# Optimization experiments

Measured on AMD Instinct MI355X. Metric: run time of the kernel, lower is better.

The kernel has to match this reference:

```python
import jax, jax.numpy as jnp
import numpy as np
from jax import lax

N = 200; E = 3200; HID = 64; NH = 16; OUT = 2 * HID; CAT = NH * OUT  # CAT = 2048
ALPHA = 0.2


def _gat(h, e_attr, adj, n2n, W, a_s, a_d, a_e, We, concat):
    # edge-feature-aware GAT head: logits from Wh_i, Wh_j and projected node2node feats
    Nn = h.shape[0]
    Wh = h @ W                                       # [N, out]
    ee = ((n2n @ We) @ a_e).reshape(Nn, Nn)          # [N, N] edge-feature term
    logits = jax.nn.leaky_relu((Wh @ a_s)[:, None] + (Wh @ a_d)[None, :] + ee,
                               negative_slope=ALPHA)
    logits = jnp.where(adj > 0, logits, -1e9)        # mask to graph structure
    att = jax.nn.softmax(logits, axis=1)
    h2 = att @ Wh
    if concat:
        h2 = jax.nn.elu(h2)
    return h2, jax.nn.elu(e_attr @ We)               # updated node + edge features


def _edge_pool(x, eidx, e, w, b):
    # static-shape edge pooling: score edges, gate nodes by mean incident score
    src, dst = eidx[0], eidx[1]
    s = jax.nn.sigmoid(jnp.concatenate([x[src], x[dst], e], axis=1) @ w + b)  # [E]
    deg = jax.ops.segment_sum(jnp.ones_like(s), src, num_segments=x.shape[0])
    ns = jax.ops.segment_sum(s, src, num_segments=x.shape[0]) / (deg + 1e-6)
    return x * ns[:, None], e * s[:, None]


def _gpool(x, w, b):
    # GlobalAttention: gate_nn = Linear+Sigmoid, softmax over nodes, weighted sum
    gate = jax.nn.softmax(jax.nn.sigmoid(x @ w + b), axis=0)  # [N, 1]
    return jnp.sum(gate * x, axis=0, keepdims=True)           # [1, D]


def _adj_n2n(Nn, eidx, eattr):
    # vectorized version of the per-edge Python loop in _get_adj_node2node
    src, dst = eidx[0], eidx[1]
    adj = jnp.zeros((Nn, Nn), eattr.dtype).at[src, dst].set(1.0)
    n2n = jnp.zeros((Nn * Nn, eattr.shape[1]), eattr.dtype).at[src * Nn + dst].set(eattr)
    return adj, n2n


def _lstm_dir(x, Wih, Whh, b):
    # one LSTM direction over seq x [T, Din] (PyTorch i,f,g,o gate order)
    Hh = Whh.shape[1]
    def step(carry, xt):
        h, c = carry
        g = xt @ Wih.T + h @ Whh.T + b
        i, f, gg, o = jnp.split(g, 4)
        c = jax.nn.sigmoid(f) * c + jax.nn.sigmoid(i) * jnp.tanh(gg)
        h = jax.nn.sigmoid(o) * jnp.tanh(c)
        return (h, c), h
    (_, _), ys = lax.scan(step, (jnp.zeros(Hh, x.dtype), jnp.zeros(Hh, x.dtype)), x)
    return ys


def setup_inputs():
    key = jax.random.key(0)
    ks = iter(jax.random.split(key, 64))
    def rn(shape, scale=0.05):
        return jax.random.normal(next(ks), shape, jnp.float32) * scale
    inp = {}
    for g in (1, 2):
        eidx = jax.random.randint(next(ks), (2, E), 0, N)
        eattr = rn((E, HID), 1.0)
        adj, n2n = _adj_n2n(N, eidx, eattr)
        inp['features%d' % g] = rn((N, HID), 1.0)
        inp['edge_index%d' % g] = eidx
        inp['edgesAttr%d' % g] = eattr
        inp['adjacency%d' % g] = adj
        inp['node2node%d' % g] = n2n
    inp.update(dict(
        W_h=rn((HID, HID)),
        W_gat=rn((NH, HID, OUT)), a_src=rn((NH, OUT)), a_dst=rn((NH, OUT)),
        a_e=rn((NH, OUT)), We_gat=rn((NH, HID, OUT)),
        W_out=rn((CAT, OUT)), ao_src=rn((OUT,)), ao_dst=rn((OUT,)), ao_e=rn((OUT,)),
        We_out=rn((CAT, OUT)),
        ep1_w=rn((3 * CAT,)), ep1_b=rn(()),
        ep2_w=rn((3 * OUT,)), ep2_b=rn(()),
        g1_w=rn((HID, 1)), g1_b=rn((1,)),
        g2_w=rn((CAT, 1)), g2_b=rn((1,)),
        g3_w=rn((OUT, 1)), g3_b=rn((1,)),
        Wih0=rn((2, 512, 35 * HID)), Whh0=rn((2, 512, 128)), b0=rn((2, 512)),
        Wih1=rn((2, 512, 256)), Whh1=rn((2, 512, 128)), b1=rn((2, 512)),
        fc_w=rn((256, 2)), fc_b=rn((2,)),
    ))
    return inp


def reference(features1, features2, edge_index1, edge_index2, edgesAttr1, edgesAttr2,
              adjacency1, adjacency2, node2node1, node2node2,
              W_h, W_gat, a_src, a_dst, a_e, We_gat,
              W_out, ao_src, ao_dst, ao_e, We_out,
              ep1_w, ep1_b, ep2_w, ep2_b,
              g1_w, g1_b, g2_w, g2_b, g3_w, g3_b,
              Wih0, Whh0, b0, Wih1, Whh1, b1, fc_w, fc_b):
    def graph(feat, eidx, eattr, adj, n2n):
        h = jax.nn.elu(feat @ W_h)                              # SingleNodeAttentionLayer
        hs = [_gpool(h, g1_w, g1_b)]
        outs = [_gat(h, eattr, adj, n2n, W_gat[i], a_src[i], a_dst[i], a_e[i],
                     We_gat[i], True) for i in range(NH)]
        h = jnp.concatenate([o[0] for o in outs], axis=1)       # [N, 2048]
        eattr = jnp.concatenate([o[1] for o in outs], axis=1)   # [E, 2048]
        h, eattr = _edge_pool(h, eidx, eattr, ep1_w, ep1_b)
        hs.append(_gpool(h, g2_w, g2_b))
        adj2, n2n2 = _adj_n2n(h.shape[0], eidx, eattr)          # dense [N*N, 2048]
        h, eattr = _gat(h, eattr, adj2, n2n2, W_out, ao_src, ao_dst, ao_e, We_out, False)
        h, eattr = _edge_pool(h, eidx, eattr, ep2_w, ep2_b)
        hs.append(_gpool(h, g3_w, g3_b))
        return jnp.concatenate(hs, axis=1)                      # [1, 35*HID]

    h1 = graph(features1, edge_index1, edgesAttr1, adjacency1, node2node1)
    h2 = graph(features2, edge_index2, edgesAttr2, adjacency2, node2node2)
    x = jnp.concatenate([h1, h2], axis=0)                       # seq [2, 2240]
    for Wih, Whh, b in ((Wih0, Whh0, b0), (Wih1, Whh1, b1)):
        f = _lstm_dir(x, Wih[0], Whh[0], b[0])
        r = _lstm_dir(x[::-1], Wih[1], Whh[1], b[1])[::-1]
        x = jnp.concatenate([f, r], axis=1)                     # [2, 256]
    logits = x[-1] @ fc_w + fc_b
    return jax.nn.softmax(logits)[None, :]                      # [1, nclass]
```

## Files before the change

### kernel.cpp

```cpp
#include <hip/hip_runtime.h>
#include <math.h>

#define DI static __device__ __forceinline__

DI float eluf(float x){ return x > 0.f ? x : expm1f(x); }
DI float lreluf(float x){ return x > 0.f ? x : 0.2f*x; }
DI float sigmf(float x){ return 1.f/(1.f+expf(-x)); }

typedef unsigned short u16;
typedef unsigned int   u32;
typedef __attribute__((ext_vector_type(8))) short short8_t;
typedef __attribute__((ext_vector_type(4))) float f32x4;

DI u16 bf16rne(float f){
  u32 u = __float_as_uint(f);
  u += 0x7fffu + ((u>>16)&1u);
  return (u16)(u>>16);
}

DI f32x4 bmfma(short8_t a, short8_t b, f32x4 c){
  return __builtin_amdgcn_mfma_f32_16x16x32_bf16(a, b, c, 0, 0, 0);
}

constexpr int N=200, E=3200, HID=64, NH=16, OUTD=128, CAT=2048, SEQD=2240;

constexpr int OH0   = 0;
constexpr int OWH   = OH0 + N*HID;
constexpr int OASN  = OWH + NH*N*OUTD;
constexpr int OADN  = OASN + NH*N;
constexpr int OH1   = OADN + NH*N;
constexpr int OXW1  = OH1 + N*CAT;
constexpr int OXW2  = OXW1 + 256;
constexpr int OEW1  = OXW2 + 256;
constexpr int OS1   = OEW1 + E;
constexpr int ODEG1 = OS1 + E;
constexpr int OSS1  = ODEG1 + 256;
constexpr int ORAW1 = OSS1 + 256;
constexpr int OWH2  = ORAW1 + 256;
constexpr int OAS2  = OWH2 + N*OUTD;
constexpr int OAD2  = OAS2 + 256;
constexpr int OEWV  = OAD2 + 256;
constexpr int OH2B  = OEWV + E;
constexpr int OXS2  = OH2B + N*OUTD;
constexpr int OXD2  = OXS2 + 256;
constexpr int ODEG2 = OXD2 + 256;
constexpr int OSS2  = ODEG2 + 256;
constexpr int ORAW2 = OSS2 + 256;
constexpr int ORAW3 = ORAW2 + 256;
constexpr int PGF   = ORAW3 + 256;
constexpr int GLOBF = 10624;
constexpr int TOTF  = GLOBF + 2*PGF;

__device__ __attribute__((aligned(16))) float G_F[TOTF];
__device__ float G_E2PART[(size_t)4*2*E*OUTD];
__device__ float G_EDOTH[2*NH*E];
__device__ float G_WHHT[2*2*128*512];
__device__ int   G_PIDX[2*N*N];
__device__ __attribute__((aligned(16))) u16 G_WGAT_T[NH*OUTD*HID];
__device__ __attribute__((aligned(16))) u16 G_WOUT_T[OUTD*CAT];
__device__ __attribute__((aligned(16))) u16 G_EATTR_BF[2*E*HID];

DI float* gf(int g){ return G_F + GLOBF + (size_t)g*PGF; }
DI float* gwe_ae(){ return G_F; }
DI float* gv_e(){ return G_F + 1024; }
DI float* gy0(){ return G_F + 3072; }
DI float* gy1(){ return G_F + 3584; }
DI float* gxseq(){ return G_F + 4096; }
DI float* gxg(){ return G_F + 8576; }
DI int*   gpidx(int g){ return G_PIDX + g*N*N; }

struct GraphIn {
  const float *feat, *eattr, *adj, *n2n;
  const int   *eidx;
};

struct Params {
  GraphIn g[2];
  const float *W_h, *W_gat, *a_src, *a_dst, *a_e, *We_gat;
  const float *W_out, *ao_src, *ao_dst, *ao_e, *We_out;
  const float *ep1_w, *ep1_b, *ep2_w, *ep2_b;
  const float *g1_w, *g1_b, *g2_w, *g2_b, *g3_w, *g3_b;
  const float *Wih0, *Whh0, *b0, *Wih1, *Whh1, *b1, *fc_w, *fc_b;
  float *out;
};

constexpr int ZPG  = 2*E + 1024;
constexpr int IB_Z = (2*ZPG+255)/256;
constexpr int IB_C = (2*N*N+255)/256;
constexpr int IB_D = (2*2*512*128)/256;
constexpr int IB_E = (NH*HID+CAT+3)/4;
constexpr int IB_H = (2*N+3)/4;
constexpr int IB_W1 = (NH*OUTD*HID)/256;
constexpr int IB_W2 = (OUTD*CAT)/256;
constexpr int IB_EA = (2*E*HID)/256;
__global__ void k_init(Params P){
  int b = blockIdx.x, tid = threadIdx.x;
  if (b < IB_Z){
    int i = b*256 + tid;
    if (i < 2*ZPG){
      int g = i/ZPG, r = i%ZPG;
      int addr = r<E ? OEW1+r : (r<2*E ? OEWV+(r-E) :
                 (r<2*E+512 ? ODEG1+(r-2*E) : ODEG2+(r-2*E-512)));
      gf(g)[addr] = 0.f;
    }
  } else if (b < IB_Z+IB_C){
    int i = (b-IB_Z)*256 + tid; if (i < 2*N*N) G_PIDX[i] = -1;
  } else if (b < IB_Z+IB_C+IB_D){
    int idx = (b-IB_Z-IB_C)*256 + tid;
    int l = idx >> 17;
    int r = idx & 131071;
    int d = r >> 16;
    int r2 = r & 65535;
    int gate = r2 & 511;
    int k = r2 >> 9;
    const float* Whh = l ? P.Whh1 : P.Whh0;
    G_WHHT[idx] = Whh[((size_t)d*512+gate)*128 + k];
  } else if (b < IB_Z+IB_C+IB_D+IB_E){
    int gid = (b-IB_Z-IB_C-IB_D)*4 + (tid>>6);
    int lane = tid & 63;
    if (gid < NH*HID){
      int h = gid/HID, c = gid%HID;
      const float* W = P.We_gat + (size_t)(h*HID+c)*OUTD;
      const float* a = P.a_e + h*OUTD;
      float acc = 0.f;
      for (int o=lane;o<OUTD;o+=64) acc += W[o]*a[o];
      for (int off=32;off>0;off>>=1) acc += __shfl_down(acc,off);
      if (lane==0) gwe_ae()[gid] = acc;
    } else if (gid < NH*HID+CAT){
      int c = gid - NH*HID;
      const float* W = P.We_out + (size_t)c*OUTD;
      float acc = 0.f;
      for (int o=lane;o<OUTD;o+=64) acc += W[o]*P.ao_e[o];
      for (int off=32;off>0;off>>=1) acc += __shfl_down(acc,off);
      if (lane==0) gv_e()[c] = acc;
    }
  } else if (b < IB_Z+IB_C+IB_D+IB_E+IB_H){
    int unit = (b-IB_Z-IB_C-IB_D-IB_E)*4 + (tid>>6);
    if (unit >= 2*N) return;
    int g = unit / N, n = unit % N, c = tid & 63;
    const float* feat = P.g[g].feat;
    float acc = 0.f;
    for (int k=0;k<HID;k++) acc += feat[n*HID+k]*P.W_h[k*HID+c];
    float v = eluf(acc);
    float* f = gf(g);
    f[OH0 + n*HID + c] = v;
    float r = v*P.g1_w[c];
    for (int off=32;off>0;off>>=1) r += __shfl_down(r,off);
    if (c==0) f[ORAW1+n] = r;
  } else if (b < IB_Z+IB_C+IB_D+IB_E+IB_H+IB_W1){
    int i = (b-(IB_Z+IB_C+IB_D+IB_E+IB_H))*256 + tid;
    int h = i>>13, o = (i>>6)&127, c = i&63;
    G_WGAT_T[i] = bf16rne(P.We_gat[(size_t)(h*HID+c)*OUTD + o]);
  } else if (b < IB_Z+IB_C+IB_D+IB_E+IB_H+IB_W1+IB_W2){
    int i = (b-(IB_Z+IB_C+IB_D+IB_E+IB_H+IB_W1))*256 + tid;
    int n = i>>11, q = i&2047;
    G_WOUT_T[i] = bf16rne(P.We_out[(size_t)q*OUTD + n]);
  } else {
    int i = (b-(IB_Z+IB_C+IB_D+IB_E+IB_H+IB_W1+IB_W2))*256 + tid;
    int g = i >= E*HID ? 1 : 0;
    G_EATTR_BF[i] = bf16rne(P.g[g].eattr[i - g*E*HID]);
  }
}

__global__ void k_edoth(Params P){
  int b = blockIdx.x, tid = threadIdx.x;
  int g = b / (E/16);
  int e0 = (b % (E/16)) * 16;
  __shared__ float ea[16][HID+1];
  __shared__ float wa[16][HID+1];
  {
    int row = tid >> 4, c0 = (tid & 15)*4;
    float4 v = *(const float4*)&P.g[g].eattr[(size_t)(e0+row)*HID + c0];
    ea[row][c0]=v.x; ea[row][c0+1]=v.y; ea[row][c0+2]=v.z; ea[row][c0+3]=v.w;
    float4 w = *(const float4*)&gwe_ae()[row*HID + c0];
    wa[row][c0]=w.x; wa[row][c0+1]=w.y; wa[row][c0+2]=w.z; wa[row][c0+3]=w.w;
  }
  __syncthreads();
  int h = tid >> 4, el = tid & 15;
  float acc = 0.f;
  #pragma unroll
  for (int c=0;c<HID;c++) acc += ea[el][c]*wa[h][c];
  G_EDOTH[((size_t)g*NH + h)*E + e0 + el] = acc;
}

__global__ void k_Wh(Params P){
  int n = blockIdx.x, h = blockIdx.y, g = blockIdx.z, o = threadIdx.x;
  float* f = gf(g);
  if (h == NH){
    if (n != 0) return;
    __shared__ float att[N];
    __shared__ float sb[128];
    for (int j = o; j < N; j += 128) att[j] = sigmf(f[ORAW1+j] + P.g1_b[0]);
    __syncthreads();
    float m = -3e38f;
    for (int j = o; j < N; j += 128) m = fmaxf(m, att[j]);
    sb[o] = m; __syncthreads();
    for (int s=64;s>0;s>>=1){ if (o<s) sb[o]=fmaxf(sb[o],sb[o+s]); __syncthreads(); }
    m = sb[0]; __syncthreads();
    float ss = 0.f;
    for (int j = o; j < N; j += 128){ float e = expf(att[j]-m); ss += e; }
    sb[o] = ss; __syncthreads();
    for (int s=64;s>0;s>>=1){ if (o<s) sb[o]+=sb[o+s]; __syncthreads(); }
    float inv = 1.f/sb[0]; __syncthreads();
    for (int j = o; j < N; j += 128) att[j] = expf(att[j]-m)*inv;
    __syncthreads();
    if (o < HID){
      float acc = 0.f;
      for (int j=0;j<N;j++) acc += att[j]*f[OH0 + j*HID + o];
      gxseq()[g*SEQD + o] = acc;
    }
    return;
  }
  __shared__ float hs[HID];
  __shared__ float sred[128], dred[128];
  if (o < HID) hs[o] = f[OH0 + n*HID + o];
  __syncthreads();
  const float* W = P.W_gat + (size_t)h*HID*OUTD + o;
  float acc = 0.f;
  for (int c=0;c<HID;c++) acc += hs[c]*W[(size_t)c*OUTD];
  f[OWH + ((size_t)h*N + n)*OUTD + o] = acc;
  sred[o] = acc*P.a_src[h*OUTD+o];
  dred[o] = acc*P.a_dst[h*OUTD+o];
  __syncthreads();
  for (int s=64;s>0;s>>=1){ if (o<s){ sred[o]+=sred[o+s]; dred[o]+=dred[o+s]; } __syncthreads(); }
  if (o==0){ f[OASN+h*N+n]=sred[0]; f[OADN+h*N+n]=dred[0]; }
}

__global__ void k_att1(Params P){
  int nb = blockIdx.x, h = blockIdx.y, g = blockIdx.z, tid = threadIdx.x;
  int n0 = nb*4;
  __shared__ float z[4][N];
  __shared__ float red[128];
  __shared__ float sinv[4];
  float* f = gf(g);
  const float* adj = P.g[g].adj;
  const int* pidx = gpidx(g);
  const float* edoth = G_EDOTH + ((size_t)g*NH + h)*E;
  const float* adn = f + OADN + h*N;
  for (int i=0;i<4;i++){
    float asn = f[OASN + h*N + n0+i];
    for (int j = tid; j < N; j += 128){
      float a = adj[(n0+i)*N + j];
      float zz;
      if (a > 0.f){
        int p = pidx[(n0+i)*N + j];
        float ee = (p >= 0) ? edoth[p] : 0.f;
        zz = lreluf(asn + adn[j] + ee);
      } else zz = -1e9f;
      z[i][j] = zz;
    }
  }
  __syncthreads();
  for (int i=0;i<4;i++){
    float m = -3e38f;
    for (int j = tid; j < N; j += 128) m = fmaxf(m, z[i][j]);
    red[tid] = m; __syncthreads();
    for (int s=64;s>0;s>>=1){ if (tid<s) red[tid]=fmaxf(red[tid],red[tid+s]); __syncthreads(); }
    m = red[0]; __syncthreads();
    float ssum = 0.f;
    for (int j = tid; j < N; j += 128){ float e = expf(z[i][j]-m); z[i][j]=e; ssum += e; }
    red[tid] = ssum; __syncthreads();
    for (int s=64;s>0;s>>=1){ if (tid<s) red[tid]+=red[tid+s]; __syncthreads(); }
    if (tid==0) sinv[i] = 1.f/red[0];
    __syncthreads();
  }
  const float* wh = f + OWH + (size_t)h*N*OUTD;
  float a0=0.f,a1=0.f,a2=0.f,a3=0.f;
  for (int j=0;j<N;j++){
    float w = wh[(size_t)j*OUTD + tid];
    a0 += z[0][j]*w; a1 += z[1][j]*w; a2 += z[2][j]*w; a3 += z[3][j]*w;
  }
  f[OH1 + (size_t)(n0+0)*CAT + h*OUTD + tid] = eluf(a0*sinv[0]);
  f[OH1 + (size_t)(n0+1)*CAT + h*OUTD + tid] = eluf(a1*sinv[1]);
  f[OH1 + (size_t)(n0+2)*CAT + h*OUTD + tid] = eluf(a2*sinv[2]);
  f[OH1 + (size_t)(n0+3)*CAT + h*OUTD + tid] = eluf(a3*sinv[3]);
}

__global__ void k_xw1(Params P){
  int n = blockIdx.x, g = blockIdx.y, tid = threadIdx.x;
  __shared__ float s1b[256], s2b[256], s3b[256];
  float* f = gf(g);
  const float* x = f + OH1 + (size_t)n*CAT;
  float a1 = 0.f, a2 = 0.f, a3 = 0.f;
  for (int c = tid; c < CAT; c += 256){
    float xv = x[c];
    a1 += xv*P.ep1_w[c];
    a2 += xv*P.ep1_w[CAT+c];
    a3 += xv*P.g2_w[c];
  }
  s1b[tid]=a1; s2b[tid]=a2; s3b[tid]=a3; __syncthreads();
  for (int s=128;s>0;s>>=1){
    if (tid<s){ s1b[tid]+=s1b[tid+s]; s2b[tid]+=s2b[tid+s]; s3b[tid]+=s3b[tid+s]; }
    __syncthreads();
  }
  if (tid==0){ f[OXW1+n]=s1b[0]; f[OXW2+n]=s2b[0]; f[ORAW2+n]=s3b[0]; }
}

__global__ void k_s1(Params P){
  int e = blockIdx.x*256 + threadIdx.x, g = blockIdx.y;
  if (e >= E) return;
  float* f = gf(g);
  const int* ei = P.g[g].eidx;
  int s = ei[e], d = ei[E+e];
  float v = sigmf(f[OXW1+s] + f[OXW2+d] + f[OEW1+e] + P.ep1_b[0]);
  f[OS1+e] = v;
  atomicAdd(&f[OSS1+s], v);
  atomicAdd(&f[ODEG1+s], 1.f);
}

__global__ void k_pairs(Params P){
  int e = blockIdx.x*256 + threadIdx.x, g = blockIdx.y;
  if (e >= E) return;
  const int* ei = P.g[g].eidx;
  atomicMax(&gpidx(g)[ei[e]*N + ei[E+e]], e);
}

__global__ void k_gpool_out(Params P, int xoff, int D, int odeg, int rawoff,
                            const float* b, int outoff){
  int cb = blockIdx.x, g = blockIdx.y, tid = threadIdx.x;
  __shared__ float att[N];
  __shared__ float sb[256];
  float* f = gf(g);
  for (int n = tid; n < N; n += 256){
    float sc = f[odeg+256+n]/(f[odeg+n]+1e-6f);
    att[n] = sigmf(f[rawoff+n]*sc + b[0]);
  }
  __syncthreads();
  float m = -3e38f;
  for (int n = tid; n < N; n += 256) m = fmaxf(m, att[n]);
  sb[tid] = m; __syncthreads();
  for (int s=128;s>0;s>>=1){ if (tid<s) sb[tid]=fmaxf(sb[tid],sb[tid+s]); __syncthreads(); }
  m = sb[0]; __syncthreads();
  float ss = 0.f;
  for (int n = tid; n < N; n += 256){ float e = expf(att[n]-m); ss += e; }
  sb[tid] = ss; __syncthreads();
  for (int s=128;s>0;s>>=1){ if (tid<s) sb[tid]+=sb[tid+s]; __syncthreads(); }
  float inv = 1.f/sb[0]; __syncthreads();
  for (int n = tid; n < N; n += 256){
    float sc = f[odeg+256+n]/(f[odeg+n]+1e-6f);
    att[n] = expf(att[n]-m)*inv*sc;
  }
  __syncthreads();
  int c = cb*256 + tid;
  if (c < D){
    const float* x = f + xoff;
    float acc = 0.f;
    for (int n=0;n<N;n++) acc += att[n]*x[(size_t)n*D + c];
    gxseq()[g*SEQD + outoff + c] = acc;
  }
}

__global__ void k_Wh2(Params P){
  int n = blockIdx.x, g = blockIdx.y, tid = threadIdx.x;
  int kq = tid >> 7, o = tid & 127;
  __shared__ float hrow[4][128];
  __shared__ float part[4][128];
  __shared__ float sr[128], dr[128];
  float* f = gf(g);
  const float* x = f + OH1 + (size_t)n*CAT;
  float acc = 0.f;
  for (int cc=0; cc<4; cc++){
    int c0 = kq*512 + cc*128;
    __syncthreads();
    hrow[kq][o] = x[c0 + o];
    __syncthreads();
    const float* W = P.W_out + (size_t)c0*OUTD + o;
    for (int j=0;j<128;j++) acc += hrow[kq][j]*W[(size_t)j*OUTD];
  }
  part[kq][o] = acc;
  __syncthreads();
  if (kq==0){
    float ns = f[OSS1+n]/(f[ODEG1+n]+1e-6f);
    float a = part[0][o]+part[1][o]+part[2][o]+part[3][o];
    float v = a*ns;
    f[OWH2 + (size_t)n*OUTD + o] = v;
    sr[o] = v*P.ao_src[o];
    dr[o] = v*P.ao_dst[o];
  }
  __syncthreads();
  for (int s=64;s>0;s>>=1){
    if (tid<s){ sr[tid]+=sr[tid+s]; dr[tid]+=dr[tid+s]; }
    __syncthreads();
  }
  if (tid==0){ f[OAS2+n]=sr[0]; f[OAD2+n]=dr[0]; }
}

__global__ void k_att2(Params P){
  int n = blockIdx.x, g = blockIdx.y, tid = threadIdx.x;
  __shared__ float z[N];
  __shared__ float red[128];
  __shared__ float dred[128];
  __shared__ float gred[128];
  float* f = gf(g);
  const float* adj = P.g[g].adj;
  const int* pidx = gpidx(g);
  float asn = f[OAS2+n];
  const float* adn = f + OAD2;
  for (int j = tid; j < N; j += 128){
    float a = adj[n*N + j];
    float zz;
    if (a > 0.f){
      int p = pidx[n*N + j];
      float ee = (p >= 0) ? f[OEWV+p]*f[OS1+p] : 0.f;
      zz = lreluf(asn + adn[j] + ee);
    } else zz = -1e9f;
    z[j] = zz;
  }
  __syncthreads();
  float m = -3e38f;
  for (int j = tid; j < N; j += 128) m = fmaxf(m, z[j]);
  red[tid] = m; __syncthreads();
  for (int s=64;s>0;s>>=1){ if (tid<s) red[tid]=fmaxf(red[tid],red[tid+s]); __syncthreads(); }
  m = red[0]; __syncthreads();
  float ssum = 0.f;
  for (int j = tid; j < N; j += 128){ float e = expf(z[j]-m); z[j]=e; ssum += e; }
  red[tid] = ssum; __syncthreads();
  for (int s=64;s>0;s>>=1){ if (tid<s) red[tid]+=red[tid+s]; __syncthreads(); }
  float inv = 1.f/red[0]; __syncthreads();
  const float* wh = f + OWH2;
  float acc = 0.f;
  for (int j=0;j<N;j++){
    float w = z[j];
    if (w != 0.f) acc += w * wh[(size_t)j*OUTD + tid];
  }
  float v = acc*inv;
  f[OH2B + (size_t)n*OUTD + tid] = v;
  red[tid]  = v*P.ep2_w[tid];
  dred[tid] = v*P.ep2_w[OUTD+tid];
  gred[tid] = v*P.g3_w[tid];
  __syncthreads();
  for (int s=64;s>0;s>>=1){
    if (tid<s){ red[tid]+=red[tid+s]; dred[tid]+=dred[tid+s]; gred[tid]+=gred[tid+s]; }
    __syncthreads();
  }
  if (tid==0){ f[OXS2+n]=red[0]; f[OXD2+n]=dred[0]; f[ORAW3+n]=gred[0]; }
}

__global__ __launch_bounds__(256) void k_e2p_mfma(Params P){
  int eb = blockIdx.x, hg = blockIdx.y, g = blockIdx.z;
  int tid = threadIdx.x;
  int wave = tid>>6, lane = tid&63, l16 = lane&15, l4 = lane>>4;
  __shared__ __attribute__((aligned(16))) u16 Tlds[32*512];
  int e0 = eb*32;
  int nt0 = wave*2;
  const u16* ea = G_EATTR_BF + ((size_t)g*E + e0)*HID;
  short8_t af00 = *(const short8_t*)(ea + l16*HID + l4*8);
  short8_t af01 = *(const short8_t*)(ea + l16*HID + 32 + l4*8);
  short8_t af10 = *(const short8_t*)(ea + (16+l16)*HID + l4*8);
  short8_t af11 = *(const short8_t*)(ea + (16+l16)*HID + 32 + l4*8);
  float ew1p0[4] = {0.f,0.f,0.f,0.f}, ewvp0[4] = {0.f,0.f,0.f,0.f};
  float ew1p1[4] = {0.f,0.f,0.f,0.f}, ewvp1[4] = {0.f,0.f,0.f,0.f};
  for (int hh=0; hh<4; hh++){
    int h = hg*4 + hh;
    const u16* Wg = G_WGAT_T + (size_t)h*OUTD*HID;
    #pragma unroll
    for (int nn=0; nn<2; nn++){
      int nt = nt0 + nn;
      const u16* Wgn = Wg + (size_t)(nt*16 + l16)*HID + l4*8;
      short8_t wg0 = *(const short8_t*)Wgn;
      short8_t wg1 = *(const short8_t*)(Wgn + 32);
      f32x4 d0 = {0.f,0.f,0.f,0.f}, d1 = {0.f,0.f,0.f,0.f};
      d0 = bmfma(af00, wg0, d0);
      d1 = bmfma(af10, wg0, d1);
      d0 = bmfma(af01, wg1, d0);
      d1 = bmfma(af11, wg1, d1);
      int qg = h*OUTD + nt*16 + l16;
      float w1 = P.ep1_w[2*CAT + qg];
      float wv = gv_e()[qg];
      int qloc = hh*128 + nt*16 + l16;
      #pragma unroll
      for (int r=0;r<4;r++){
        float v0 = d0[r] > 0.f ? d0[r] : expm1f(d0[r]);
        float v1 = d1[r] > 0.f ? d1[r] : expm1f(d1[r]);
        ew1p0[r] += v0*w1; ewvp0[r] += v0*wv;
        ew1p1[r] += v1*w1; ewvp1[r] += v1*wv;
        int row = l4*4 + r;
        int byt = (row*1024 + qloc*2) ^ ((row&7)<<4);
        *(u16*)((char*)Tlds + byt) = bf16rne(v0);
        *(u16*)((char*)Tlds + byt + 16384) = bf16rne(v1);
      }
    }
  }
  const u16* WoA = G_WOUT_T + (size_t)(wave*32 + l16)*CAT + hg*512 + l4*8;
  const u16* WoB = WoA + 16*CAT;
  short8_t w0a = *(const short8_t*)WoA;
  short8_t w0b = *(const short8_t*)WoB;
  short8_t w1a = *(const short8_t*)(WoA + 32);
  short8_t w1b = *(const short8_t*)(WoB + 32);
  float* f = gf(g);
  #pragma unroll
  for (int r=0;r<4;r++){
    float a0 = ew1p0[r], b0 = ewvp0[r], a1 = ew1p1[r], b1 = ewvp1[r];
    a0 += __shfl_xor(a0,1); b0 += __shfl_xor(b0,1); a1 += __shfl_xor(a1,1); b1 += __shfl_xor(b1,1);
    a0 += __shfl_xor(a0,2); b0 += __shfl_xor(b0,2); a1 += __shfl_xor(a1,2); b1 += __shfl_xor(b1,2);
    a0 += __shfl_xor(a0,4); b0 += __shfl_xor(b0,4); a1 += __shfl_xor(a1,4); b1 += __shfl_xor(b1,4);
    a0 += __shfl_xor(a0,8); b0 += __shfl_xor(b0,8); a1 += __shfl_xor(a1,8); b1 += __shfl_xor(b1,8);
    if (l16==0){
      int e = e0 + l4*4 + r;
      atomicAdd(&f[OEW1+e], a0);
      atomicAdd(&f[OEWV+e], b0);
      atomicAdd(&f[OEW1+e+16], a1);
      atomicAdd(&f[OEWV+e+16], b1);
    }
  }
  __syncthreads();
  f32x4 acc00 = {0.f,0.f,0.f,0.f}, acc01 = {0.f,0.f,0.f,0.f};
  f32x4 acc10 = {0.f,0.f,0.f,0.f}, acc11 = {0.f,0.f,0.f,0.f};
  #pragma unroll
  for (int ks=0; ks<16; ks++){
    short8_t na = w0a, nb = w0b;
    if (ks < 14){
      na = *(const short8_t*)(WoA + (ks+2)*32);
      nb = *(const short8_t*)(WoB + (ks+2)*32);
    }
    int byt = (l16*1024 + ks*64 + l4*16) ^ ((l16&7)<<4);
    short8_t a0 = *(const short8_t*)((const char*)Tlds + byt);
    short8_t a1 = *(const short8_t*)((const char*)Tlds + byt + 16384);
    acc00 = bmfma(a0, w0a, acc00);
    acc10 = bmfma(a1, w0a, acc10);
    acc01 = bmfma(a0, w0b, acc01);
    acc11 = bmfma(a1, w0b, acc11);
    w0a = w1a; w0b = w1b; w1a = na; w1b = nb;
  }
  float* dst = G_E2PART + (((size_t)hg*2 + g)*E + e0)*OUTD;
  #pragma unroll
  for (int r=0;r<4;r++){
    int ee = l4*4 + r;
    dst[(size_t)ee*OUTD + wave*32 + l16]      = acc00[r];
    dst[(size_t)ee*OUTD + wave*32 + 16 + l16] = acc01[r];
    dst[(size_t)(16+ee)*OUTD + wave*32 + l16]      = acc10[r];
    dst[(size_t)(16+ee)*OUTD + wave*32 + 16 + l16] = acc11[r];
  }
}

constexpr int TE2 = 16;
__global__ void k_ew2fin(Params P){
  int e0 = blockIdx.x*TE2, g = blockIdx.y, tid = threadIdx.x;
  __shared__ float lred[2][TE2];
  float* f = gf(g);
  float w2 = P.ep2_w[2*OUTD + tid];
  int lane = tid & 63, wvi = tid >> 6;
  for (int e=0;e<TE2;e++){
    const float* src = G_E2PART + ((size_t)g*E + e0 + e)*OUTD + tid;
    float a = 0.f;
    for (int h=0;h<4;h++) a += src[(size_t)h*2*E*OUTD];
    float v = eluf(f[OS1+e0+e]*a) * w2;
    for (int off=32;off>0;off>>=1) v += __shfl_down(v,off);
    if (lane==0) lred[wvi][e]=v;
  }
  __syncthreads();
  if (tid < TE2){
    int e = e0 + tid;
    float ew2 = lred[0][tid]+lred[1][tid];
    const int* ei = P.g[g].eidx;
    int s = ei[e], d = ei[E+e];
    float v = sigmf(f[OXS2+s] + f[OXD2+d] + ew2 + P.ep2_b[0]);
    atomicAdd(&f[OSS2+s], v);
    atomicAdd(&f[ODEG2+s], 1.f);
  }
}

__global__ void k_lstm_xg(Params P, int layer){
  int gid = blockIdx.x*4 + (threadIdx.x>>6);
  int lane = threadIdx.x & 63;
  int t = gid >> 10;
  int rem = gid & 1023;
  int d = rem >> 9;
  int gate = rem & 511;
  const float* Wih = layer ? P.Wih1 : P.Wih0;
  const float* bb  = layer ? P.b1   : P.b0;
  const float* xin = layer ? gy0()  : gxseq();
  int Din = layer ? 256 : SEQD;
  const float* x = xin + t*Din;
  const float* Wr = Wih + ((size_t)d*512 + gate)*Din;
  float acc = 0.f;
  for (int k=lane; k<Din; k+=64) acc += x[k]*Wr[k];
  for (int off=32; off>0; off>>=1) acc += __shfl_down(acc, off);
  if (lane==0) gxg()[(t*2 + d)*512 + gate] = acc + bb[d*512 + gate];
}

__global__ void k_lstm_rec(Params P, int layer){
  int d = blockIdx.x, tid = threadIdx.x;
  float* yout = layer ? gy1() : gy0();
  const float* T = G_WHHT + (size_t)(layer*2 + d)*128*512;
  __shared__ float h[128], c[128], gbuf[512];
  if (tid < 128){ h[tid]=0.f; c[tid]=0.f; }
  __syncthreads();
  for (int s=0;s<2;s++){
    int t = (d==0) ? s : 1-s;
    float acc = gxg()[(t*2 + d)*512 + tid];
    for (int k=0;k<128;k++) acc += h[k]*T[(size_t)k*512 + tid];
    gbuf[tid] = acc;
    __syncthreads();
    if (tid < 128){
      float ii = sigmf(gbuf[tid]);
      float ff = sigmf(gbuf[128+tid]);
      float gg = tanhf(gbuf[256+tid]);
      float oo = sigmf(gbuf[384+tid]);
      float cn = ff*c[tid] + ii*gg;
      c[tid] = cn;
      float hn = oo*tanhf(cn);
      h[tid] = hn;
      yout[t*256 + d*128 + tid] = hn;
    }
    __syncthreads();
  }
}

__global__ void k_final(Params P){
  int tid = threadIdx.x;
  __shared__ float sb[256], sb2[256];
  const float* x = gy1() + 256;
  sb[tid]  = x[tid]*P.fc_w[tid*2+0];
  sb2[tid] = x[tid]*P.fc_w[tid*2+1];
  __syncthreads();
  for (int s=128;s>0;s>>=1){ if (tid<s){ sb[tid]+=sb[tid+s]; sb2[tid]+=sb2[tid+s]; } __syncthreads(); }
  if (tid==0){
    float l0 = sb[0] + P.fc_b[0];
    float l1 = sb2[0] + P.fc_b[1];
    float m = fmaxf(l0,l1);
    float e0 = expf(l0-m), e1 = expf(l1-m), inv = 1.f/(e0+e1);
    P.out[0] = e0*inv;
    P.out[1] = e1*inv;
  }
}

extern "C" void kernel_launch(void* const* d_in, const int* in_sizes, int n_in,
                              void* d_out, int out_size, void* d_ws, size_t ws_size,
                              hipStream_t stream){
  Params P;
  for (int g=0; g<2; ++g){
    int b = g*5;
    P.g[g].feat  = (const float*)d_in[b+0];
    P.g[g].eidx  = (const int*)d_in[b+1];
    P.g[g].eattr = (const float*)d_in[b+2];
    P.g[g].adj   = (const float*)d_in[b+3];
    P.g[g].n2n   = (const float*)d_in[b+4];
  }
  P.W_h   = (const float*)d_in[10];
  P.W_gat = (const float*)d_in[11];
  P.a_src = (const float*)d_in[12];
  P.a_dst = (const float*)d_in[13];
  P.a_e   = (const float*)d_in[14];
  P.We_gat= (const float*)d_in[15];
  P.W_out = (const float*)d_in[16];
  P.ao_src= (const float*)d_in[17];
  P.ao_dst= (const float*)d_in[18];
  P.ao_e  = (const float*)d_in[19];
  P.We_out= (const float*)d_in[20];
  P.ep1_w = (const float*)d_in[21];
  P.ep1_b = (const float*)d_in[22];
  P.ep2_w = (const float*)d_in[23];
  P.ep2_b = (const float*)d_in[24];
  P.g1_w  = (const float*)d_in[25];
  P.g1_b  = (const float*)d_in[26];
  P.g2_w  = (const float*)d_in[27];
  P.g2_b  = (const float*)d_in[28];
  P.g3_w  = (const float*)d_in[29];
  P.g3_b  = (const float*)d_in[30];
  P.Wih0  = (const float*)d_in[31];
  P.Whh0  = (const float*)d_in[32];
  P.b0    = (const float*)d_in[33];
  P.Wih1  = (const float*)d_in[34];
  P.Whh1  = (const float*)d_in[35];
  P.b1    = (const float*)d_in[36];
  P.fc_w  = (const float*)d_in[37];
  P.fc_b  = (const float*)d_in[38];
  P.out   = (float*)d_out;

  k_init <<<dim3(IB_Z+IB_C+IB_D+IB_E+IB_H+IB_W1+IB_W2+IB_EA), 256, 0, stream>>>(P);
  k_pairs<<<dim3((E+255)/256,2), 256, 0, stream>>>(P);
  k_edoth<<<dim3(2*(E/16)), 256, 0, stream>>>(P);
  k_e2p_mfma<<<dim3(E/32, 4, 2), 256, 0, stream>>>(P);
  k_Wh   <<<dim3(N,NH+1,2), 128, 0, stream>>>(P);
  k_att1 <<<dim3(N/4,NH,2),128, 0, stream>>>(P);
  k_xw1  <<<dim3(N,2),    256, 0, stream>>>(P);
  k_s1   <<<dim3((E+255)/256,2), 256, 0, stream>>>(P);
  k_gpool_out<<<dim3(8,2), 256, 0, stream>>>(P, OH1, CAT, ODEG1, ORAW2, P.g2_b, HID);
  k_Wh2  <<<dim3(N,2),    512, 0, stream>>>(P);
  k_att2 <<<dim3(N,2),    128, 0, stream>>>(P);
  k_ew2fin<<<dim3(E/TE2,2),128, 0, stream>>>(P);
  k_gpool_out<<<dim3(1,2), 256, 0, stream>>>(P, OH2B, OUTD, ODEG2, ORAW3, P.g3_b, HID+CAT);

  k_lstm_xg <<<dim3(512), 256, 0, stream>>>(P, 0);
  k_lstm_rec<<<dim3(2),   512, 0, stream>>>(P, 0);
  k_lstm_xg <<<dim3(512), 256, 0, stream>>>(P, 1);
  k_lstm_rec<<<dim3(2),   512, 0, stream>>>(P, 1);
  k_final<<<dim3(1), 256, 0, stream>>>(P);
}
```

Baseline: 367.6 us.

## Fuse edge-dot-head computation into MFMA kernel and split heads finer

Removes the separate k_edoth kernel and the precomputed We·a_e vectors. The MFMA edge kernel now accumulates the per-head edge attention term from its projected edge features, with atomic adds into a zero-initialised buffer. The same kernel also processes 2 heads per block instead of 4, doubling grid parallelism and halving shared memory, and preloads all Wout fragments into registers. The cost is twice as many partial buffers for the final reduction, extra atomics, and edge logits now derived from bf16-rounded inputs.

```diff
diff --git a/kernel.cpp b/kernel.cpp
--- a/kernel.cpp
+++ b/kernel.cpp
@@ -52,7 +52,7 @@
 constexpr int TOTF  = GLOBF + 2*PGF;
 
 __device__ __attribute__((aligned(16))) float G_F[TOTF];
-__device__ float G_E2PART[(size_t)4*2*E*OUTD];
+__device__ float G_E2PART[(size_t)8*2*E*OUTD];
 __device__ float G_EDOTH[2*NH*E];
 __device__ float G_WHHT[2*2*128*512];
 __device__ int   G_PIDX[2*N*N];
@@ -61,7 +61,6 @@
 __device__ __attribute__((aligned(16))) u16 G_EATTR_BF[2*E*HID];
 
 DI float* gf(int g){ return G_F + GLOBF + (size_t)g*PGF; }
-DI float* gwe_ae(){ return G_F; }
 DI float* gv_e(){ return G_F + 1024; }
 DI float* gy0(){ return G_F + 3072; }
 DI float* gy1(){ return G_F + 3584; }
@@ -84,11 +83,11 @@
   float *out;
 };
 
-constexpr int ZPG  = 2*E + 1024;
+constexpr int ZPG  = 2*E + 1024 + NH*E;
 constexpr int IB_Z = (2*ZPG+255)/256;
 constexpr int IB_C = (2*N*N+255)/256;
 constexpr int IB_D = (2*2*512*128)/256;
-constexpr int IB_E = (NH*HID+CAT+3)/4;
+constexpr int IB_E = (CAT+3)/4;
 constexpr int IB_H = (2*N+3)/4;
 constexpr int IB_W1 = (NH*OUTD*HID)/256;
 constexpr int IB_W2 = (OUTD*CAT)/256;
@@ -99,9 +98,13 @@
     int i = b*256 + tid;
     if (i < 2*ZPG){
       int g = i/ZPG, r = i%ZPG;
-      int addr = r<E ? OEW1+r : (r<2*E ? OEWV+(r-E) :
-                 (r<2*E+512 ? ODEG1+(r-2*E) : ODEG2+(r-2*E-512)));
-      gf(g)[addr] = 0.f;
+      if (r < 2*E+1024){
+        int addr = r<E ? OEW1+r : (r<2*E ? OEWV+(r-E) :
+                   (r<2*E+512 ? ODEG1+(r-2*E) : ODEG2+(r-2*E-512)));
+        gf(g)[addr] = 0.f;
+      } else {
+        G_EDOTH[(size_t)g*NH*E + (r - (2*E+1024))] = 0.f;
+      }
     }
   } else if (b < IB_Z+IB_C){
     int i = (b-IB_Z)*256 + tid; if (i < 2*N*N) G_PIDX[i] = -1;
@@ -118,21 +121,12 @@
   } else if (b < IB_Z+IB_C+IB_D+IB_E){
     int gid = (b-IB_Z-IB_C-IB_D)*4 + (tid>>6);
     int lane = tid & 63;
-    if (gid < NH*HID){
-      int h = gid/HID, c = gid%HID;
-      const float* W = P.We_gat + (size_t)(h*HID+c)*OUTD;
-      const float* a = P.a_e + h*OUTD;
-      float acc = 0.f;
-      for (int o=lane;o<OUTD;o+=64) acc += W[o]*a[o];
-      for (int off=32;off>0;off>>=1) acc += __shfl_down(acc,off);
-      if (lane==0) gwe_ae()[gid] = acc;
-    } else if (gid < NH*HID+CAT){
-      int c = gid - NH*HID;
-      const float* W = P.We_out + (size_t)c*OUTD;
+    if (gid < CAT){
+      const float* W = P.We_out + (size_t)gid*OUTD;
       float acc = 0.f;
       for (int o=lane;o<OUTD;o+=64) acc += W[o]*P.ao_e[o];
       for (int off=32;off>0;off>>=1) acc += __shfl_down(acc,off);
-      if (lane==0) gv_e()[c] = acc;
+      if (lane==0) gv_e()[gid] = acc;
     }
   } else if (b < IB_Z+IB_C+IB_D+IB_E+IB_H){
     int unit = (b-IB_Z-IB_C-IB_D-IB_E)*4 + (tid>>6);
@@ -162,27 +156,6 @@
   }
 }
 
-__global__ void k_edoth(Params P){
-  int b = blockIdx.x, tid = threadIdx.x;
-  int g = b / (E/16);
-  int e0 = (b % (E/16)) * 16;
-  __shared__ float ea[16][HID+1];
-  __shared__ float wa[16][HID+1];
-  {
-    int row = tid >> 4, c0 = (tid & 15)*4;
-    float4 v = *(const float4*)&P.g[g].eattr[(size_t)(e0+row)*HID + c0];
-    ea[row][c0]=v.x; ea[row][c0+1]=v.y; ea[row][c0+2]=v.z; ea[row][c0+3]=v.w;
-    float4 w = *(const float4*)&gwe_ae()[row*HID + c0];
-    wa[row][c0]=w.x; wa[row][c0+1]=w.y; wa[row][c0+2]=w.z; wa[row][c0+3]=w.w;
-  }
-  __syncthreads();
-  int h = tid >> 4, el = tid & 15;
-  float acc = 0.f;
-  #pragma unroll
-  for (int c=0;c<HID;c++) acc += ea[el][c]*wa[h][c];
-  G_EDOTH[((size_t)g*NH + h)*E + e0 + el] = acc;
-}
-
 __global__ void k_Wh(Params P){
   int n = blockIdx.x, h = blockIdx.y, g = blockIdx.z, o = threadIdx.x;
   float* f = gf(g);
@@ -440,7 +413,7 @@
   int eb = blockIdx.x, hg = blockIdx.y, g = blockIdx.z;
   int tid = threadIdx.x;
   int wave = tid>>6, lane = tid&63, l16 = lane&15, l4 = lane>>4;
-  __shared__ __attribute__((aligned(16))) u16 Tlds[32*512];
+  __shared__ __attribute__((aligned(16))) u16 Tlds[32*256];
   int e0 = eb*32;
   int nt0 = wave*2;
   const u16* ea = G_EATTR_BF + ((size_t)g*E + e0)*HID;
@@ -448,49 +421,65 @@
   short8_t af01 = *(const short8_t*)(ea + l16*HID + 32 + l4*8);
   short8_t af10 = *(const short8_t*)(ea + (16+l16)*HID + l4*8);
   short8_t af11 = *(const short8_t*)(ea + (16+l16)*HID + 32 + l4*8);
-  float ew1p0[4] = {0.f,0.f,0.f,0.f}, ewvp0[4] = {0.f,0.f,0.f,0.f};
-  float ew1p1[4] = {0.f,0.f,0.f,0.f}, ewvp1[4] = {0.f,0.f,0.f,0.f};
-  for (int hh=0; hh<4; hh++){
-    int h = hg*4 + hh;
-    const u16* Wg = G_WGAT_T + (size_t)h*OUTD*HID;
+  short8_t wg[2][2][2];
+  #pragma unroll
+  for (int hh=0; hh<2; hh++){
+    const u16* Wg = G_WGAT_T + (size_t)(hg*2+hh)*OUTD*HID;
+    #pragma unroll
+    for (int nn=0; nn<2; nn++){
+      const u16* Wgn = Wg + (size_t)((nt0+nn)*16 + l16)*HID + l4*8;
+      wg[hh][nn][0] = *(const short8_t*)Wgn;
+      wg[hh][nn][1] = *(const short8_t*)(Wgn + 32);
+    }
+  }
+  float ew1p[2][4], ewvp[2][4], edp[2][2][4];
+  #pragma unroll
+  for (int t=0;t<2;t++)
+    #pragma unroll
+    for (int r=0;r<4;r++){ ew1p[t][r]=0.f; ewvp[t][r]=0.f; edp[0][t][r]=0.f; edp[1][t][r]=0.f; }
+  #pragma unroll
+  for (int hh=0; hh<2; hh++){
+    int h = hg*2 + hh;
     #pragma unroll
     for (int nn=0; nn<2; nn++){
       int nt = nt0 + nn;
-      const u16* Wgn = Wg + (size_t)(nt*16 + l16)*HID + l4*8;
-      short8_t wg0 = *(const short8_t*)Wgn;
-      short8_t wg1 = *(const short8_t*)(Wgn + 32);
       f32x4 d0 = {0.f,0.f,0.f,0.f}, d1 = {0.f,0.f,0.f,0.f};
-      d0 = bmfma(af00, wg0, d0);
-      d1 = bmfma(af10, wg0, d1);
-      d0 = bmfma(af01, wg1, d0);
-      d1 = bmfma(af11, wg1, d1);
+      d0 = bmfma(af00, wg[hh][nn][0], d0);
+      d1 = bmfma(af10, wg[hh][nn][0], d1);
+      d0 = bmfma(af01, wg[hh][nn][1], d0);
+      d1 = bmfma(af11, wg[hh][nn][1], d1);
       int qg = h*OUTD + nt*16 + l16;
+      float ae = P.a_e[qg];
       float w1 = P.ep1_w[2*CAT + qg];
       float wv = gv_e()[qg];
       int qloc = hh*128 + nt*16 + l16;
       #pragma unroll
       for (int r=0;r<4;r++){
+        edp[hh][0][r] += d0[r]*ae;
+        edp[hh][1][r] += d1[r]*ae;
         float v0 = d0[r] > 0.f ? d0[r] : expm1f(d0[r]);
         float v1 = d1[r] > 0.f ? d1[r] : expm1f(d1[r]);
-        ew1p0[r] += v0*w1; ewvp0[r] += v0*wv;
-        ew1p1[r] += v1*w1; ewvp1[r] += v1*wv;
+        ew1p[0][r] += v0*w1; ewvp[0][r] += v0*wv;
+        ew1p[1][r] += v1*w1; ewvp[1][r] += v1*wv;
         int row = l4*4 + r;
-        int byt = (row*1024 + qloc*2) ^ ((row&7)<<4);
+        int byt = (row*512 + qloc*2) ^ ((row&7)<<4);
         *(u16*)((char*)Tlds + byt) = bf16rne(v0);
-        *(u16*)((char*)Tlds + byt + 16384) = bf16rne(v1);
+        *(u16*)((char*)Tlds + byt + 8192) = bf16rne(v1);
       }
     }
   }
-  const u16* WoA = G_WOUT_T + (size_t)(wave*32 + l16)*CAT + hg*512 + l4*8;
+  const u16* WoA = G_WOUT_T + (size_t)(wave*32 + l16)*CAT + hg*256 + l4*8;
   const u16* WoB = WoA + 16*CAT;
-  short8_t w0a = *(const short8_t*)WoA;
-  short8_t w0b = *(const short8_t*)WoB;
-  short8_t w1a = *(const short8_t*)(WoA + 32);
-  short8_t w1b = *(const short8_t*)(WoB + 32);
+  short8_t woa[8], wob[8];
+  #pragma unroll
+  for (int ks=0; ks<8; ks++){
+    woa[ks] = *(const short8_t*)(WoA + ks*32);
+    wob[ks] = *(const short8_t*)(WoB + ks*32);
+  }
   float* f = gf(g);
   #pragma unroll
   for (int r=0;r<4;r++){
-    float a0 = ew1p0[r], b0 = ewvp0[r], a1 = ew1p1[r], b1 = ewvp1[r];
+    float a0 = ew1p[0][r], b0 = ewvp[0][r], a1 = ew1p[1][r], b1 = ewvp[1][r];
     a0 += __shfl_xor(a0,1); b0 += __shfl_xor(b0,1); a1 += __shfl_xor(a1,1); b1 += __shfl_xor(b1,1);
     a0 += __shfl_xor(a0,2); b0 += __shfl_xor(b0,2); a1 += __shfl_xor(a1,2); b1 += __shfl_xor(b1,2);
     a0 += __shfl_xor(a0,4); b0 += __shfl_xor(b0,4); a1 += __shfl_xor(a1,4); b1 += __shfl_xor(b1,4);
@@ -503,24 +492,34 @@
       atomicAdd(&f[OEWV+e+16], b1);
     }
   }
+  #pragma unroll
+  for (int hh=0; hh<2; hh++){
+    float* eo = G_EDOTH + ((size_t)g*NH + hg*2 + hh)*E + e0;
+    #pragma unroll
+    for (int r=0;r<4;r++){
+      float c0 = edp[hh][0][r], c1 = edp[hh][1][r];
+      c0 += __shfl_xor(c0,1); c1 += __shfl_xor(c1,1);
+      c0 += __shfl_xor(c0,2); c1 += __shfl_xor(c1,2);
+      c0 += __shfl_xor(c0,4); c1 += __shfl_xor(c1,4);
+      c0 += __shfl_xor(c0,8); c1 += __shfl_xor(c1,8);
+      if (l16==0){
+        atomicAdd(&eo[l4*4 + r], c0);
+        atomicAdd(&eo[16 + l4*4 + r], c1);
+      }
+    }
+  }
   __syncthreads();
   f32x4 acc00 = {0.f,0.f,0.f,0.f}, acc01 = {0.f,0.f,0.f,0.f};
   f32x4 acc10 = {0.f,0.f,0.f,0.f}, acc11 = {0.f,0.f,0.f,0.f};
   #pragma unroll
-  for (int ks=0; ks<16; ks++){
-    short8_t na = w0a, nb = w0b;
-    if (ks < 14){
-      na = *(const short8_t*)(WoA + (ks+2)*32);
-      nb = *(const short8_t*)(WoB + (ks+2)*32);
-    }
-    int byt = (l16*1024 + ks*64 + l4*16) ^ ((l16&7)<<4);
+  for (int ks=0; ks<8; ks++){
+    int byt = (l16*512 + ks*64 + l4*16) ^ ((l16&7)<<4);
     short8_t a0 = *(const short8_t*)((const char*)Tlds + byt);
-    short8_t a1 = *(const short8_t*)((const char*)Tlds + byt + 16384);
-    acc00 = bmfma(a0, w0a, acc00);
-    acc10 = bmfma(a1, w0a, acc10);
-    acc01 = bmfma(a0, w0b, acc01);
-    acc11 = bmfma(a1, w0b, acc11);
-    w0a = w1a; w0b = w1b; w1a = na; w1b = nb;
+    short8_t a1 = *(const short8_t*)((const char*)Tlds + byt + 8192);
+    acc00 = bmfma(a0, woa[ks], acc00);
+    acc10 = bmfma(a1, woa[ks], acc10);
+    acc01 = bmfma(a0, wob[ks], acc01);
+    acc11 = bmfma(a1, wob[ks], acc11);
   }
   float* dst = G_E2PART + (((size_t)hg*2 + g)*E + e0)*OUTD;
   #pragma unroll
@@ -543,7 +542,8 @@
   for (int e=0;e<TE2;e++){
     const float* src = G_E2PART + ((size_t)g*E + e0 + e)*OUTD + tid;
     float a = 0.f;
-    for (int h=0;h<4;h++) a += src[(size_t)h*2*E*OUTD];
+    #pragma unroll
+    for (int h=0;h<8;h++) a += src[(size_t)h*2*E*OUTD];
     float v = eluf(f[OS1+e0+e]*a) * w2;
     for (int off=32;off>0;off>>=1) v += __shfl_down(v,off);
     if (lane==0) lred[wvi][e]=v;
@@ -670,8 +670,7 @@
 
   k_init <<<dim3(IB_Z+IB_C+IB_D+IB_E+IB_H+IB_W1+IB_W2+IB_EA), 256, 0, stream>>>(P);
   k_pairs<<<dim3((E+255)/256,2), 256, 0, stream>>>(P);
-  k_edoth<<<dim3(2*(E/16)), 256, 0, stream>>>(P);
-  k_e2p_mfma<<<dim3(E/32, 4, 2), 256, 0, stream>>>(P);
+  k_e2p_mfma<<<dim3(E/32, 8, 2), 256, 0, stream>>>(P);
   k_Wh   <<<dim3(N,NH+1,2), 128, 0, stream>>>(P);
   k_att1 <<<dim3(N/4,NH,2),128, 0, stream>>>(P);
   k_xw1  <<<dim3(N,2),    256, 0, stream>>>(P);
```

Result: slower. 378.8 us (+3.0%).
